# Kernel optimization log

Hardware: AMD Instinct MI355X
Metric: run time of the kernel (lower is better)

The kernel has to match this reference:

```python
import jax, jax.numpy as jnp
import numpy as np

DIM = 384
NUM_HEADS = 12
WS = 7
POSMLP_DIM = 32
HEAD_DIM = DIM // NUM_HEADS
SCALE = HEAD_DIM ** -0.5


def setup_inputs() -> dict:
    key = jax.random.key(0)
    ks = jax.random.split(key, 10)
    B_ = 2048
    N = WS * WS
    nW = 64
    inp = {
        "x": jax.random.normal(ks[0], (B_, N, DIM), dtype=jnp.float32),
        "mask": jax.random.normal(ks[1], (nW, N, N), dtype=jnp.float32),
        # qkv Linear: weight [3*dim, dim], bias [3*dim]
        "qkv_w": jax.random.normal(ks[2], (3 * DIM, DIM), dtype=jnp.float32) * (DIM ** -0.5),
        "qkv_b": jax.random.normal(ks[3], (3 * DIM,), dtype=jnp.float32) * 0.02,
        # proj Linear
        "proj_w": jax.random.normal(ks[4], (DIM, DIM), dtype=jnp.float32) * (DIM ** -0.5),
        "proj_b": jax.random.normal(ks[5], (DIM,), dtype=jnp.float32) * 0.02,
        # posmlp: Conv2d(2, posmlp_dim, 1) -> ReLU -> Conv2d(posmlp_dim, num_heads, 1)
        "pm_w1": jax.random.normal(ks[6], (POSMLP_DIM, 2), dtype=jnp.float32) * 0.5,
        "pm_b1": jax.random.normal(ks[7], (POSMLP_DIM,), dtype=jnp.float32) * 0.02,
        "pm_w2": jax.random.normal(ks[8], (NUM_HEADS, POSMLP_DIM), dtype=jnp.float32) * (POSMLP_DIM ** -0.5),
        "pm_b2": jax.random.normal(ks[9], (NUM_HEADS,), dtype=jnp.float32) * 0.02,
    }
    return inp


def _pos_bias(pm_w1, pm_b1, pm_w2, pm_b2):
    # pos_hw: [2, N] with channel 0 = row index, channel 1 = col index
    coords = jnp.arange(WS, dtype=jnp.float32)
    pos_h = jnp.repeat(coords[:, None], WS, axis=1).reshape(-1)  # row idx
    pos_w = jnp.tile(coords[None, :], (WS, 1)).reshape(-1)       # col idx
    pos = jnp.stack([pos_h, pos_w], axis=0)                      # [2, N]
    # pos_input[c, i, j] = pos[c, j] - pos[c, i]  (unsqueeze(2) - unsqueeze(3))
    d = pos[:, None, :] - pos[:, :, None]                        # [2, N, N]
    d = jnp.sign(d) * jnp.log1p(jnp.abs(d))
    # 1x1 convs == per-position channel MLP
    h = jax.nn.relu(jnp.einsum("cij,oc->oij", d, pm_w1) + pm_b1[:, None, None])
    bias = jnp.einsum("cij,oc->oij", h, pm_w2) + pm_b2[:, None, None]  # [H, N, N]
    return bias


def reference(x, mask, qkv_w, qkv_b, proj_w, proj_b, pm_w1, pm_b1, pm_w2, pm_b2):
    B_, N, C = x.shape
    H = NUM_HEADS
    qkv = x @ qkv_w.T + qkv_b                                     # [B_, N, 3C]
    qkv = qkv.reshape(B_, N, 3, H, C // H).transpose(2, 0, 3, 1, 4)
    q, k, v = qkv[0], qkv[1], qkv[2]                              # [B_, H, N, d]
    attn = jnp.einsum("bhnd,bhmd->bhnm", q * SCALE, k)            # [B_, H, N, N]
    attn = attn + _pos_bias(pm_w1, pm_b1, pm_w2, pm_b2)[None]
    nW = mask.shape[0]
    attn = attn.reshape(B_ // nW, nW, H, N, N) + mask[None, :, None]
    attn = jax.nn.softmax(attn.reshape(B_, H, N, N), axis=-1)
    out = jnp.einsum("bhnm,bhmd->bhnd", attn, v)                  # [B_, H, N, d]
    out = out.transpose(0, 2, 1, 3).reshape(B_, N, C)
    return out @ proj_w.T + proj_b
```

## Files before the change

kernel.cpp:

```cpp
#include <hip/hip_runtime.h>
#include <hip/hip_bf16.h>
#include <stdint.h>

#define DIM 384
#define QKVN 1152
#define NHEAD 12
#define HDIM 32
#define NTOK 49
#define NWIN 2048
static constexpr float SCALE_Q = 0.17677669529663687f;

typedef float f32x4 __attribute__((ext_vector_type(4)));
typedef __bf16 bf16x8 __attribute__((ext_vector_type(8)));
typedef unsigned short u16;
typedef u16 u16x8 __attribute__((ext_vector_type(8)));
typedef u16 u16x4 __attribute__((ext_vector_type(4)));

static __device__ __forceinline__ u16 f2bf(float f) {
  __hip_bfloat16 h = __float2bfloat16(f);
  return __builtin_bit_cast(unsigned short, h);
}
static __device__ __forceinline__ f32x4 mfma_bf16(u16x8 a, u16x8 b, f32x4 c) {
  return __builtin_amdgcn_mfma_f32_16x16x32_bf16(
      __builtin_bit_cast(bf16x8, a), __builtin_bit_cast(bf16x8, b), c, 0, 0, 0);
}

__global__ void k_convert(const float* __restrict__ s, u16* __restrict__ d, int n) {
  int i = (blockIdx.x * 256 + threadIdx.x) * 4;
  if (i < n) {
    float4 v = *(const float4*)(s + i);
    u16x4 o;
    o[0] = f2bf(v.x); o[1] = f2bf(v.y); o[2] = f2bf(v.z); o[3] = f2bf(v.w);
    *(u16x4*)(d + i) = o;
  }
}

__global__ void k_posbias(const float* __restrict__ w1, const float* __restrict__ b1,
                          const float* __restrict__ w2, const float* __restrict__ b2,
                          float* __restrict__ out) {
  int idx = blockIdx.x * 256 + threadIdx.x;
  if (idx >= NTOK * NTOK) return;
  int i = idx / NTOK, j = idx % NTOK;
  float d0 = (float)(j / 7 - i / 7);
  float d1 = (float)(j % 7 - i % 7);
  d0 = copysignf(log1pf(fabsf(d0)), d0);
  d1 = copysignf(log1pf(fabsf(d1)), d1);
  float acc[NHEAD];
#pragma unroll
  for (int o2 = 0; o2 < NHEAD; o2++) acc[o2] = b2[o2];
#pragma unroll 4
  for (int o = 0; o < 32; o++) {
    float h = fmaxf(d0 * w1[o * 2] + d1 * w1[o * 2 + 1] + b1[o], 0.f);
#pragma unroll
    for (int o2 = 0; o2 < NHEAD; o2++) acc[o2] += h * w2[o2 * 32 + o];
  }
#pragma unroll
  for (int o2 = 0; o2 < NHEAD; o2++) out[(o2 * NTOK + i) * NTOK + j] = acc[o2];
}

__global__ void k_pbm(const float* __restrict__ posb, const float* __restrict__ mask,
                      float* __restrict__ pbm) {
  int idx = blockIdx.x * 256 + threadIdx.x;
  if (idx >= 64 * NHEAD * NTOK * NTOK) return;
  int j = idx % (NTOK * NTOK);
  int t = idx / (NTOK * NTOK);
  int h = t % NHEAD, w = t / NHEAD;
  pbm[idx] = posb[h * NTOK * NTOK + j] + mask[w * NTOK * NTOK + j];
}

template <int MODE>
__global__ __launch_bounds__(256) void k_gemm(const void* __restrict__ Ap,
                                              const u16* __restrict__ Bw,
                                              const float* __restrict__ bias,
                                              void* __restrict__ Cp) {
  __shared__ u16 As[128 * 32];
  __shared__ u16 Bs[128 * 32];
  const int tid = threadIdx.x;
  const int NB = (MODE == 0) ? 9 : 3;
  const int PER = (MODE == 0) ? 882 : 294;
  const int g = blockIdx.x;
  const int flat = (g & 7) * PER + (g >> 3);
  const int bm = flat / NB, bn = flat % NB;

  const int lane = tid & 63, wv = tid >> 6;
  const int wr = wv >> 1, wc = wv & 1;
  const int l15 = lane & 15, l4 = lane >> 4;
  const int srow = tid >> 1, sp = tid & 1;
  const int fS = (srow >> 1) & 3;
  const int ws0 = (2 * sp) ^ fS, ws1 = (2 * sp + 1) ^ fS;
  const int fr = (l15 >> 1) & 3;
  f32x4 acc[4][4] = {};

  for (int k0 = 0; k0 < DIM; k0 += 32) {
    u16x8 aval0, aval1;
    if (MODE == 0) {
      const float* ap = (const float*)Ap + (size_t)(bm * 128 + srow) * DIM + k0 + sp * 16;
      float4 f0 = *(const float4*)(ap);
      float4 f1 = *(const float4*)(ap + 4);
      float4 f2 = *(const float4*)(ap + 8);
      float4 f3 = *(const float4*)(ap + 12);
      aval0[0] = f2bf(f0.x); aval0[1] = f2bf(f0.y); aval0[2] = f2bf(f0.z); aval0[3] = f2bf(f0.w);
      aval0[4] = f2bf(f1.x); aval0[5] = f2bf(f1.y); aval0[6] = f2bf(f1.z); aval0[7] = f2bf(f1.w);
      aval1[0] = f2bf(f2.x); aval1[1] = f2bf(f2.y); aval1[2] = f2bf(f2.z); aval1[3] = f2bf(f2.w);
      aval1[4] = f2bf(f3.x); aval1[5] = f2bf(f3.y); aval1[6] = f2bf(f3.z); aval1[7] = f2bf(f3.w);
    } else {
      const u16* ap = (const u16*)Ap + (size_t)(bm * 128 + srow) * DIM + k0 + sp * 16;
      aval0 = *(const u16x8*)ap;
      aval1 = *(const u16x8*)(ap + 8);
    }
    const u16* bp = Bw + (size_t)(bn * 128 + srow) * DIM + k0 + sp * 16;
    u16x8 bval0 = *(const u16x8*)bp;
    u16x8 bval1 = *(const u16x8*)(bp + 8);

    __syncthreads();
    *(u16x8*)&As[srow * 32 + ws0 * 8] = aval0;
    *(u16x8*)&As[srow * 32 + ws1 * 8] = aval1;
    *(u16x8*)&Bs[srow * 32 + ws0 * 8] = bval0;
    *(u16x8*)&Bs[srow * 32 + ws1 * 8] = bval1;
    __syncthreads();

    u16x8 af[4], bfr[4];
#pragma unroll
    for (int m = 0; m < 4; m++)
      af[m] = *(const u16x8*)&As[(wr * 64 + m * 16 + l15) * 32 + (l4 ^ fr) * 8];
#pragma unroll
    for (int n = 0; n < 4; n++)
      bfr[n] = *(const u16x8*)&Bs[(wc * 64 + n * 16 + l15) * 32 + (l4 ^ fr) * 8];
#pragma unroll
    for (int m = 0; m < 4; m++)
#pragma unroll
      for (int n = 0; n < 4; n++)
        acc[m][n] = mfma_bf16(af[m], bfr[n], acc[m][n]);
  }

#pragma unroll
  for (int n = 0; n < 4; n++) {
    const int col = bn * 128 + wc * 64 + n * 16 + l15;
    const float bv = bias[col];
#pragma unroll
    for (int m = 0; m < 4; m++) {
      const int row0 = bm * 128 + wr * 64 + m * 16 + l4 * 4;
#pragma unroll
      for (int r = 0; r < 4; r++) {
        float v = acc[m][n][r] + bv;
        if (MODE == 0) {
          if (col < DIM) v *= SCALE_Q;
          ((u16*)Cp)[(size_t)(row0 + r) * QKVN + col] = f2bf(v);
        } else {
          ((float*)Cp)[(size_t)(row0 + r) * DIM + col] = v;
        }
      }
    }
  }
}

__global__ __launch_bounds__(256) void k_attn(const u16* __restrict__ qkv,
                                              const float* __restrict__ pbm,
                                              u16* __restrict__ aout) {
  __shared__ u16 qs[2][64 * 32];
  __shared__ u16 ks[2][64 * 32];
  __shared__ u16 vts[2][32 * 72];
  __shared__ u16 ps[64 * 72];
  const int g = blockIdx.x;
  const int b = (((g >> 3) >> 3) << 6) + (g & 7) * 8 + ((g >> 3) & 7);
  const int w = b & 63;
  const int tid = threadIdx.x;
  const int lane = tid & 63, wv = tid >> 6;
  const int l15 = lane & 15, l4 = lane >> 4;
  const int fr = (l15 >> 1) & 3;

  for (int i = tid; i < 64 * 32; i += 256)
    if ((i >> 5) >= NTOK) { qs[0][i] = 0; qs[1][i] = 0; ks[0][i] = 0; ks[1][i] = 0; }
  for (int i = tid; i < 32 * 72; i += 256)
    if ((i % 72) >= NTOK) { vts[0][i] = 0; vts[1][i] = 0; }

  const int trow = tid >> 2, tseg = tid & 3;
  const int fT = (trow >> 1) & 3;
  u16x8 rq, rk, rv;

#define LOAD_REGS(h)                                                              \
  if (tid < 196) {                                                                \
    const u16* src = qkv + (size_t)(b * NTOK + trow) * QKVN + (h) * HDIM + tseg * 8; \
    rq = *(const u16x8*)src;                                                      \
    rk = *(const u16x8*)(src + DIM);                                              \
    rv = *(const u16x8*)(src + 2 * DIM);                                          \
  }
#define WRITE_LDS(buf)                                                            \
  if (tid < 196) {                                                                \
    *(u16x8*)&qs[buf][trow * 32 + (tseg ^ fT) * 8] = rq;                          \
    *(u16x8*)&ks[buf][trow * 32 + (tseg ^ fT) * 8] = rk;                          \
    _Pragma("unroll") for (int j = 0; j < 8; j++)                                 \
        vts[buf][(tseg * 8 + j) * 72 + trow] = rv[j];                             \
  }

  LOAD_REGS(0)
  WRITE_LDS(0)

  for (int h = 0; h < NHEAD; ++h) {
    const int buf = h & 1;
    if (h + 1 < NHEAD) LOAD_REGS(h + 1)
    __syncthreads();

    u16x8 aq = *(const u16x8*)&qs[buf][(wv * 16 + l15) * 32 + (l4 ^ fr) * 8];
    f32x4 s[4];
#pragma unroll
    for (int n = 0; n < 4; n++) {
      u16x8 bk = *(const u16x8*)&ks[buf][(n * 16 + l15) * 32 + (l4 ^ fr) * 8];
      f32x4 z = {0.f, 0.f, 0.f, 0.f};
      s[n] = mfma_bf16(aq, bk, z);
    }

    float inv[4];
#pragma unroll
    for (int r = 0; r < 4; r++) {
      const int row = wv * 16 + l4 * 4 + r;
      const bool rok = row < NTOK;
      const float* pr = pbm + ((size_t)(w * NHEAD + h) * NTOK + (rok ? row : 0)) * NTOK;
      float sv[4];
#pragma unroll
      for (int n = 0; n < 4; n++) {
        const int col = n * 16 + l15;
        sv[n] = (col < NTOK) ? s[n][r] + pr[col] : -1e30f;
      }
      float mx = fmaxf(fmaxf(sv[0], sv[1]), fmaxf(sv[2], sv[3]));
#pragma unroll
      for (int off = 1; off < 16; off <<= 1) mx = fmaxf(mx, __shfl_xor(mx, off));
      float e[4], sum = 0.f;
#pragma unroll
      for (int n = 0; n < 4; n++) {
        const int col = n * 16 + l15;
        e[n] = (col < NTOK) ? __expf(sv[n] - mx) : 0.f;
        sum += e[n];
      }
#pragma unroll
      for (int off = 1; off < 16; off <<= 1) sum += __shfl_xor(sum, off);
      inv[r] = 1.0f / sum;
#pragma unroll
      for (int n = 0; n < 4; n++) ps[row * 72 + n * 16 + l15] = f2bf(e[n]);
    }

    f32x4 o[2] = {};
#pragma unroll
    for (int kk = 0; kk < 2; kk++) {
      u16x8 ap = *(const u16x8*)&ps[(wv * 16 + l15) * 72 + kk * 32 + l4 * 8];
#pragma unroll
      for (int n = 0; n < 2; n++) {
        u16x8 bvv = *(const u16x8*)&vts[buf][(n * 16 + l15) * 72 + kk * 32 + l4 * 8];
        o[n] = mfma_bf16(ap, bvv, o[n]);
      }
    }
#pragma unroll
    for (int n = 0; n < 2; n++) {
      const int col = n * 16 + l15;
#pragma unroll
      for (int r = 0; r < 4; r++) {
        const int row = wv * 16 + l4 * 4 + r;
        if (row < NTOK)
          aout[(size_t)(b * NTOK + row) * DIM + h * HDIM + col] = f2bf(o[n][r] * inv[r]);
      }
    }
    if (h + 1 < NHEAD) WRITE_LDS(buf ^ 1)
  }
#undef LOAD_REGS
#undef WRITE_LDS
}

extern "C" void kernel_launch(void* const* d_in, const int* in_sizes, int n_in,
                              void* d_out, int out_size, void* d_ws, size_t ws_size,
                              hipStream_t stream) {
  const float* x      = (const float*)d_in[0];
  const float* mask   = (const float*)d_in[1];
  const float* qkv_w  = (const float*)d_in[2];
  const float* qkv_b  = (const float*)d_in[3];
  const float* proj_w = (const float*)d_in[4];
  const float* proj_b = (const float*)d_in[5];
  const float* pm_w1  = (const float*)d_in[6];
  const float* pm_b1  = (const float*)d_in[7];
  const float* pm_w2  = (const float*)d_in[8];
  const float* pm_b2  = (const float*)d_in[9];
  float* out = (float*)d_out;

  char* ws = (char*)d_ws;
  u16*   qkv   = (u16*)(ws + 0);
  u16*   wqkv  = (u16*)(ws + 231211008);
  u16*   wproj = (u16*)(ws + 232095744);
  float* posb  = (float*)(ws + 232390656);
  u16*   aout  = (u16*)(ws + 232505904);
  float* pbm   = (float*)(ws + 309576240);

  k_convert<<<432, 256, 0, stream>>>(qkv_w, wqkv, 442368);
  k_convert<<<144, 256, 0, stream>>>(proj_w, wproj, 147456);
  k_posbias<<<10, 256, 0, stream>>>(pm_w1, pm_b1, pm_w2, pm_b2, posb);
  k_pbm<<<7203, 256, 0, stream>>>(posb, mask, pbm);
  k_gemm<0><<<7056, 256, 0, stream>>>((const void*)x, wqkv, qkv_b, (void*)qkv);
  k_attn<<<2048, 256, 0, stream>>>(qkv, pbm, aout);
  k_gemm<1><<<2352, 256, 0, stream>>>((const void*)aout, wproj, proj_b, (void*)out);
}
```

Measured before the change: 687.4 us.

## Prefetch next K-tile in GEMM and transpose QK^T for lane-local softmax

```diff
diff --git a/kernel.cpp b/kernel.cpp
--- a/kernel.cpp
+++ b/kernel.cpp
@@ -11,6 +11,7 @@
 static constexpr float SCALE_Q = 0.17677669529663687f;
 
 typedef float f32x4 __attribute__((ext_vector_type(4)));
+typedef float f32x4u __attribute__((ext_vector_type(4), aligned(4)));
 typedef __bf16 bf16x8 __attribute__((ext_vector_type(8)));
 typedef unsigned short u16;
 typedef u16 u16x8 __attribute__((ext_vector_type(8)));
@@ -28,9 +29,9 @@
 __global__ void k_convert(const float* __restrict__ s, u16* __restrict__ d, int n) {
   int i = (blockIdx.x * 256 + threadIdx.x) * 4;
   if (i < n) {
-    float4 v = *(const float4*)(s + i);
+    f32x4 v = *(const f32x4*)(s + i);
     u16x4 o;
-    o[0] = f2bf(v.x); o[1] = f2bf(v.y); o[2] = f2bf(v.z); o[3] = f2bf(v.w);
+    o[0] = f2bf(v[0]); o[1] = f2bf(v[1]); o[2] = f2bf(v[2]); o[3] = f2bf(v[3]);
     *(u16x4*)(d + i) = o;
   }
 }
@@ -91,33 +92,50 @@
   const int fr = (l15 >> 1) & 3;
   f32x4 acc[4][4] = {};
 
-  for (int k0 = 0; k0 < DIM; k0 += 32) {
-    u16x8 aval0, aval1;
+  f32x4 fA0, fA1, fA2, fA3;
+  u16x8 rA0, rA1, rB0, rB1;
+
+#define GLOAD(K0)                                                                   \
+  {                                                                                 \
+    if (MODE == 0) {                                                                \
+      const float* ap = (const float*)Ap + (size_t)(bm * 128 + srow) * DIM + (K0) + sp * 16; \
+      fA0 = *(const f32x4*)(ap);                                                    \
+      fA1 = *(const f32x4*)(ap + 4);                                                \
+      fA2 = *(const f32x4*)(ap + 8);                                                \
+      fA3 = *(const f32x4*)(ap + 12);                                               \
+    } else {                                                                        \
+      const u16* ap = (const u16*)Ap + (size_t)(bm * 128 + srow) * DIM + (K0) + sp * 16; \
+      rA0 = *(const u16x8*)ap;                                                      \
+      rA1 = *(const u16x8*)(ap + 8);                                                \
+    }                                                                               \
+    const u16* bp = Bw + (size_t)(bn * 128 + srow) * DIM + (K0) + sp * 16;          \
+    rB0 = *(const u16x8*)bp;                                                        \
+    rB1 = *(const u16x8*)(bp + 8);                                                  \
+  }
+
+  GLOAD(0)
+  const int NK = DIM / 32;
+  for (int it = 0; it < NK; ++it) {
+    u16x8 wa0, wa1, wb0, wb1;
     if (MODE == 0) {
-      const float* ap = (const float*)Ap + (size_t)(bm * 128 + srow) * DIM + k0 + sp * 16;
-      float4 f0 = *(const float4*)(ap);
-      float4 f1 = *(const float4*)(ap + 4);
-      float4 f2 = *(const float4*)(ap + 8);
-      float4 f3 = *(const float4*)(ap + 12);
-      aval0[0] = f2bf(f0.x); aval0[1] = f2bf(f0.y); aval0[2] = f2bf(f0.z); aval0[3] = f2bf(f0.w);
-      aval0[4] = f2bf(f1.x); aval0[5] = f2bf(f1.y); aval0[6] = f2bf(f1.z); aval0[7] = f2bf(f1.w);
-      aval1[0] = f2bf(f2.x); aval1[1] = f2bf(f2.y); aval1[2] = f2bf(f2.z); aval1[3] = f2bf(f2.w);
-      aval1[4] = f2bf(f3.x); aval1[5] = f2bf(f3.y); aval1[6] = f2bf(f3.z); aval1[7] = f2bf(f3.w);
+#pragma unroll
+      for (int j = 0; j < 4; j++) {
+        wa0[j] = f2bf(fA0[j]); wa0[j + 4] = f2bf(fA1[j]);
+        wa1[j] = f2bf(fA2[j]); wa1[j + 4] = f2bf(fA3[j]);
+      }
     } else {
-      const u16* ap = (const u16*)Ap + (size_t)(bm * 128 + srow) * DIM + k0 + sp * 16;
-      aval0 = *(const u16x8*)ap;
-      aval1 = *(const u16x8*)(ap + 8);
-    }
-    const u16* bp = Bw + (size_t)(bn * 128 + srow) * DIM + k0 + sp * 16;
-    u16x8 bval0 = *(const u16x8*)bp;
-    u16x8 bval1 = *(const u16x8*)(bp + 8);
+      wa0 = rA0; wa1 = rA1;
+    }
+    wb0 = rB0; wb1 = rB1;
 
     __syncthreads();
-    *(u16x8*)&As[srow * 32 + ws0 * 8] = aval0;
-    *(u16x8*)&As[srow * 32 + ws1 * 8] = aval1;
-    *(u16x8*)&Bs[srow * 32 + ws0 * 8] = bval0;
-    *(u16x8*)&Bs[srow * 32 + ws1 * 8] = bval1;
+    *(u16x8*)&As[srow * 32 + ws0 * 8] = wa0;
+    *(u16x8*)&As[srow * 32 + ws1 * 8] = wa1;
+    *(u16x8*)&Bs[srow * 32 + ws0 * 8] = wb0;
+    *(u16x8*)&Bs[srow * 32 + ws1 * 8] = wb1;
     __syncthreads();
+
+    if (it + 1 < NK) GLOAD((it + 1) * 32)
 
     u16x8 af[4], bfr[4];
 #pragma unroll
@@ -132,6 +150,7 @@
       for (int n = 0; n < 4; n++)
         acc[m][n] = mfma_bf16(af[m], bfr[n], acc[m][n]);
   }
+#undef GLOAD
 
 #pragma unroll
   for (int n = 0; n < 4; n++) {
@@ -178,65 +197,75 @@
   const int fT = (trow >> 1) & 3;
   u16x8 rq, rk, rv;
 
-#define LOAD_REGS(h)                                                              \
-  if (tid < 196) {                                                                \
+#define LOAD_REGS(h)                                                                 \
+  if (tid < 196) {                                                                   \
     const u16* src = qkv + (size_t)(b * NTOK + trow) * QKVN + (h) * HDIM + tseg * 8; \
-    rq = *(const u16x8*)src;                                                      \
-    rk = *(const u16x8*)(src + DIM);                                              \
-    rv = *(const u16x8*)(src + 2 * DIM);                                          \
-  }
-#define WRITE_LDS(buf)                                                            \
-  if (tid < 196) {                                                                \
-    *(u16x8*)&qs[buf][trow * 32 + (tseg ^ fT) * 8] = rq;                          \
-    *(u16x8*)&ks[buf][trow * 32 + (tseg ^ fT) * 8] = rk;                          \
-    _Pragma("unroll") for (int j = 0; j < 8; j++)                                 \
-        vts[buf][(tseg * 8 + j) * 72 + trow] = rv[j];                             \
+    rq = *(const u16x8*)src;                                                         \
+    rk = *(const u16x8*)(src + DIM);                                                 \
+    rv = *(const u16x8*)(src + 2 * DIM);                                             \
+  }
+#define WRITE_LDS(buf)                                                               \
+  if (tid < 196) {                                                                   \
+    *(u16x8*)&qs[buf][trow * 32 + (tseg ^ fT) * 8] = rq;                             \
+    *(u16x8*)&ks[buf][trow * 32 + (tseg ^ fT) * 8] = rk;                             \
+    _Pragma("unroll") for (int j = 0; j < 8; j++)                                    \
+        vts[buf][(tseg * 8 + j) * 72 + trow] = rv[j];                                \
   }
 
   LOAD_REGS(0)
   WRITE_LDS(0)
+
+  const int qrow = wv * 16 + l15;
+  const int qc = (qrow < NTOK) ? qrow : NTOK - 1;
 
   for (int h = 0; h < NHEAD; ++h) {
     const int buf = h & 1;
     if (h + 1 < NHEAD) LOAD_REGS(h + 1)
     __syncthreads();
 
-    u16x8 aq = *(const u16x8*)&qs[buf][(wv * 16 + l15) * 32 + (l4 ^ fr) * 8];
+    u16x8 bq = *(const u16x8*)&qs[buf][(wv * 16 + l15) * 32 + (l4 ^ fr) * 8];
     f32x4 s[4];
 #pragma unroll
     for (int n = 0; n < 4; n++) {
-      u16x8 bk = *(const u16x8*)&ks[buf][(n * 16 + l15) * 32 + (l4 ^ fr) * 8];
+      u16x8 ak = *(const u16x8*)&ks[buf][(n * 16 + l15) * 32 + (l4 ^ fr) * 8];
       f32x4 z = {0.f, 0.f, 0.f, 0.f};
-      s[n] = mfma_bf16(aq, bk, z);
-    }
-
-    float inv[4];
-#pragma unroll
-    for (int r = 0; r < 4; r++) {
-      const int row = wv * 16 + l4 * 4 + r;
-      const bool rok = row < NTOK;
-      const float* pr = pbm + ((size_t)(w * NHEAD + h) * NTOK + (rok ? row : 0)) * NTOK;
-      float sv[4];
-#pragma unroll
-      for (int n = 0; n < 4; n++) {
-        const int col = n * 16 + l15;
-        sv[n] = (col < NTOK) ? s[n][r] + pr[col] : -1e30f;
-      }
-      float mx = fmaxf(fmaxf(sv[0], sv[1]), fmaxf(sv[2], sv[3]));
-#pragma unroll
-      for (int off = 1; off < 16; off <<= 1) mx = fmaxf(mx, __shfl_xor(mx, off));
-      float e[4], sum = 0.f;
-#pragma unroll
-      for (int n = 0; n < 4; n++) {
-        const int col = n * 16 + l15;
-        e[n] = (col < NTOK) ? __expf(sv[n] - mx) : 0.f;
-        sum += e[n];
-      }
-#pragma unroll
-      for (int off = 1; off < 16; off <<= 1) sum += __shfl_xor(sum, off);
-      inv[r] = 1.0f / sum;
-#pragma unroll
-      for (int n = 0; n < 4; n++) ps[row * 72 + n * 16 + l15] = f2bf(e[n]);
+      s[n] = mfma_bf16(ak, bq, z);
+    }
+
+    const float* pr = pbm + ((size_t)(w * NHEAD + h) * NTOK + qc) * NTOK;
+    float sv[4][4];
+    float mx = -1e30f;
+#pragma unroll
+    for (int n = 0; n < 4; n++) {
+      f32x4 p4 = *(const f32x4u*)(pr + n * 16 + l4 * 4);
+#pragma unroll
+      for (int r = 0; r < 4; r++) {
+        const int k = n * 16 + l4 * 4 + r;
+        float v = (k < NTOK) ? s[n][r] + p4[r] : -1e30f;
+        sv[n][r] = v;
+        mx = fmaxf(mx, v);
+      }
+    }
+    mx = fmaxf(mx, __shfl_xor(mx, 16));
+    mx = fmaxf(mx, __shfl_xor(mx, 32));
+    float e[4][4], sum = 0.f;
+#pragma unroll
+    for (int n = 0; n < 4; n++)
+#pragma unroll
+      for (int r = 0; r < 4; r++) {
+        const int k = n * 16 + l4 * 4 + r;
+        e[n][r] = (k < NTOK) ? __expf(sv[n][r] - mx) : 0.f;
+        sum += e[n][r];
+      }
+    sum += __shfl_xor(sum, 16);
+    sum += __shfl_xor(sum, 32);
+    const float inv = 1.0f / sum;
+#pragma unroll
+    for (int n = 0; n < 4; n++) {
+      u16x4 pk;
+#pragma unroll
+      for (int r = 0; r < 4; r++) pk[r] = f2bf(e[n][r] * inv);
+      *(u16x4*)&ps[qrow * 72 + n * 16 + l4 * 4] = pk;
     }
 
     f32x4 o[2] = {};
@@ -256,7 +285,7 @@
       for (int r = 0; r < 4; r++) {
         const int row = wv * 16 + l4 * 4 + r;
         if (row < NTOK)
-          aout[(size_t)(b * NTOK + row) * DIM + h * HDIM + col] = f2bf(o[n][r] * inv[r]);
+          aout[(size_t)(b * NTOK + row) * DIM + h * HDIM + col] = f2bf(o[n][r]);
       }
     }
     if (h + 1 < NHEAD) WRITE_LDS(buf ^ 1)
@@ -285,8 +314,8 @@
   u16*   wqkv  = (u16*)(ws + 231211008);
   u16*   wproj = (u16*)(ws + 232095744);
   float* posb  = (float*)(ws + 232390656);
-  u16*   aout  = (u16*)(ws + 232505904);
-  float* pbm   = (float*)(ws + 309576240);
+  float* pbm   = (float*)(ws + 232505904);
+  u16*   aout  = (u16*)(ws + 239881776);
 
   k_convert<<<432, 256, 0, stream>>>(qkv_w, wqkv, 442368);
   k_convert<<<144, 256, 0, stream>>>(proj_w, wproj, 147456);
```

New measurement: 655.2 us. 4.7% less time.
